# Performance work log

Hardware: AMD Instinct MI355X
Metric: run time of the kernel (lower is better)

The kernel has to match this reference:

```python
import jax, jax.numpy as jnp
import numpy as np

N = 100000
E = 1600000
DF = 64

def setup_inputs() -> dict:
    key = jax.random.key(0)
    ks = jax.random.split(key, 8)
    y = jax.random.normal(ks[0], (N, 3), dtype=jnp.float32)
    f_y = jax.random.normal(ks[1], (N, DF), dtype=jnp.float32)
    W0 = jax.random.normal(ks[2], (6, DF), dtype=jnp.float32) * 0.1
    b0 = jnp.zeros((DF,), dtype=jnp.float32)
    W1 = jax.random.normal(ks[3], (DF, DF), dtype=jnp.float32) * 0.1
    b1 = jnp.zeros((DF,), dtype=jnp.float32)
    neighbors_index = jax.random.randint(ks[4], (E,), 0, N, dtype=jnp.int64)
    # CSR row splits: sorted random interior split points, bracketed by 0 and E
    interior = jnp.sort(jax.random.randint(ks[5], (N - 1,), 0, E, dtype=jnp.int64))
    neighbors_row_splits = jnp.concatenate([
        jnp.zeros((1,), dtype=jnp.int64), interior,
        jnp.full((1,), E, dtype=jnp.int64)])
    return {"y": y, "f_y": f_y, "W0": W0, "b0": b0, "W1": W1, "b1": b1,
            "neighbors_index": neighbors_index,
            "neighbors_row_splits": neighbors_row_splits}

def reference(y, f_y, W0, b0, W1, b1, neighbors_index, neighbors_row_splits):
    n = y.shape[0]
    e = neighbors_index.shape[0]
    # segment id of each edge (inverse of CSR row splits), == repeat_interleave
    seg = jnp.searchsorted(neighbors_row_splits, jnp.arange(e, dtype=neighbors_row_splits.dtype), side='right') - 1
    rep_features = y[neighbors_index]          # [E, d1] neighbor coords
    self_features = y[seg]                     # [E, d2] self coords (x = y)
    agg = jnp.concatenate([rep_features, self_features], axis=1)  # [E, 6]
    # MLPLinear kernel: gelu between layers, none after last (torch gelu = exact erf)
    h = jax.nn.gelu(agg @ W0 + b0, approximate=False)
    h = h @ W1 + b1                            # [E, DF]
    # transform_type 0 -> (b): k(x,y) * f(y)
    h = h * f_y[neighbors_index]
    # segment_csr mean reduction (no weights)
    sums = jax.ops.segment_sum(h, seg, num_segments=n)            # [n, DF]
    counts = (neighbors_row_splits[1:] - neighbors_row_splits[:-1]).astype(h.dtype)
    out = sums / jnp.maximum(counts, 1.0)[:, None]
    return out
```

## Files before the change

kernel.cpp:

```cpp
#include <hip/hip_runtime.h>
#include <hip/hip_bf16.h>

#define NN    100000
#define EE    1600000
#define DF    64
#define BPB   5

typedef __bf16 bf16x8 __attribute__((ext_vector_type(8)));
typedef float  f32x4  __attribute__((ext_vector_type(4)));

__device__ __forceinline__ float gelu_f(float x) {
    float u2 = x * (2.302234849f + 0.102953097f * x * x);
    float s  = exp2f(-u2);
    return __fdividef(x, 1.0f + s);
}

__device__ __forceinline__ unsigned cvt_pk_bf16(float lo, float hi) {
    unsigned r;
    asm("v_cvt_pk_bf16_f32 %0, %1, %2" : "=v"(r) : "v"(lo), "v"(hi));
    return r;
}

__global__ void it_seg(const int* __restrict__ splits, int* __restrict__ seg) {
    const int e0 = (blockIdx.x * 256 + threadIdx.x) * 2;
    int n = 0;
    #pragma unroll
    for (int step = 65536; step >= 1; step >>= 1) {
        const int cand = n + step;
        if (cand <= NN - 1 && splits[cand] <= e0) n = cand;
    }
    int2 s;
    s.x = n;
    const int e1 = e0 + 1;
    while (n < NN - 1 && splits[n + 1] <= e1) n++;
    s.y = n;
    *(int2*)(seg + e0) = s;
}

__global__ __launch_bounds__(256, 4)
void it_edge(const float* __restrict__ y, const float* __restrict__ fy,
             const float* __restrict__ W0, const float* __restrict__ b0,
             const float* __restrict__ W1, const float* __restrict__ b1,
             const int* __restrict__ nbr, const int* __restrict__ seg,
             __bf16* __restrict__ h)
{
    __shared__ __align__(16) int    nbL[4][64];
    __shared__ __align__(16) __bf16 aggW[4][64][8];
    __shared__ __align__(16) __bf16 hL[4][16][DF];

    const int t    = threadIdx.x;
    const int lane = t & 63;
    const int wv   = t >> 6;
    const int col  = lane & 15;
    const int kg   = lane >> 4;

    bf16x8 w0f[4];
    #pragma unroll
    for (int nt = 0; nt < 4; nt++)
        #pragma unroll
        for (int j = 0; j < 8; j++) {
            const int k = kg * 8 + j;
            float v = 0.0f;
            if (k < 6)       v = W0[k * DF + nt * 16 + col];
            else if (k == 6) v = b0[nt * 16 + col];
            w0f[nt][j] = (__bf16)v;
        }
    bf16x8 w1f[4][2];
    float  b1r[4];
    #pragma unroll
    for (int nt = 0; nt < 4; nt++) {
        b1r[nt] = b1[col * 4 + nt];
        #pragma unroll
        for (int kf = 0; kf < 2; kf++)
            #pragma unroll
            for (int j = 0; j < 8; j++)
                w1f[nt][kf][j] = (__bf16)W1[(kf * 32 + kg * 8 + j) * DF + col * 4 + nt];
    }

    __bf16* const hw = &hL[wv][0][0];
    const int swz = (col & 7) << 4;

    #pragma unroll 1
    for (int bb = 0; bb < BPB; bb++) {
        const int ebase = (blockIdx.x * BPB + bb) * 256 + wv * 64;
        const int e     = ebase + lane;
        const int nb    = nbr[e];
        const int sge   = seg[e];
        nbL[wv][lane] = nb;
        bf16x8 ag = {};
        ag[0] = (__bf16)y[nb * 3 + 0];
        ag[1] = (__bf16)y[nb * 3 + 1];
        ag[2] = (__bf16)y[nb * 3 + 2];
        ag[3] = (__bf16)y[sge * 3 + 0];
        ag[4] = (__bf16)y[sge * 3 + 1];
        ag[5] = (__bf16)y[sge * 3 + 2];
        ag[6] = (__bf16)1.0f;
        *(bf16x8*)&aggW[wv][lane][0] = ag;

        #pragma unroll
        for (int g = 0; g < 4; g++) {
            const int gb = g * 16;
            const int4 q = *(const int4*)&nbL[wv][gb + kg * 4];

            bf16x8 a0 = {};
            if (kg == 0) a0 = *(const bf16x8*)&aggW[wv][gb + col][0];

            f32x4 acc0[4] = {};
            #pragma unroll
            for (int nt = 0; nt < 4; nt++)
                acc0[nt] = __builtin_amdgcn_mfma_f32_16x16x32_bf16(w0f[nt], a0, acc0[nt], 0, 0, 0);

            #pragma unroll
            for (int nt = 0; nt < 4; nt++) {
                const unsigned p0 = cvt_pk_bf16(gelu_f(acc0[nt][0]), gelu_f(acc0[nt][1]));
                const unsigned p1 = cvt_pk_bf16(gelu_f(acc0[nt][2]), gelu_f(acc0[nt][3]));
                const int off = col * 128 + ((nt * 32 + kg * 8) ^ swz);
                *(int2*)((char*)hw + off) = make_int2((int)p0, (int)p1);
            }
            bf16x8 af1[2];
            #pragma unroll
            for (int kf = 0; kf < 2; kf++) {
                const int off = col * 128 + ((kf * 64 + kg * 16) ^ swz);
                af1[kf] = *(const bf16x8*)((const char*)hw + off);
            }

            f32x4 acc[4] = {};
            #pragma unroll
            for (int nt = 0; nt < 4; nt++) {
                acc[nt] = __builtin_amdgcn_mfma_f32_16x16x32_bf16(af1[0], w1f[nt][0], acc[nt], 0, 0, 0);
                acc[nt] = __builtin_amdgcn_mfma_f32_16x16x32_bf16(af1[1], w1f[nt][1], acc[nt], 0, 0, 0);
            }

            #pragma unroll
            for (int r = 0; r < 4; r++) {
                const int qq = (&q.x)[r];
                const float4 fv = *(const float4*)(fy + (size_t)qq * DF + col * 4);
                const unsigned u0 = cvt_pk_bf16((acc[0][r] + b1r[0]) * fv.x,
                                                (acc[1][r] + b1r[1]) * fv.y);
                const unsigned u1 = cvt_pk_bf16((acc[2][r] + b1r[2]) * fv.z,
                                                (acc[3][r] + b1r[3]) * fv.w);
                const size_t er = (size_t)(ebase + gb + kg * 4 + r);
                *(int2*)((char*)h + er * 128 + col * 8) = make_int2((int)u0, (int)u1);
            }
        }
    }
}

__global__ void it_reduce(const int* __restrict__ splits,
                          const __bf16* __restrict__ h,
                          float* __restrict__ out)
{
    const int t    = threadIdx.x;
    const int lane = t & 63;
    const int wv   = t >> 6;
    const int n    = blockIdx.x * 4 + wv;
    const int s0 = splits[n], s1 = splits[n + 1];
    const int par = lane >> 4;
    const int cp  = lane & 15;

    float a0 = 0.f, a1 = 0.f, a2 = 0.f, a3 = 0.f;
    for (int e = s0 + par; e < s1; e += 4) {
        const unsigned long long u =
            *(const unsigned long long*)((const char*)h + (size_t)e * 128 + cp * 8);
        const unsigned lo = (unsigned)u, hi = (unsigned)(u >> 32);
        a0 += __uint_as_float(lo << 16);
        a1 += __uint_as_float(lo & 0xffff0000u);
        a2 += __uint_as_float(hi << 16);
        a3 += __uint_as_float(hi & 0xffff0000u);
    }
    a0 += __shfl_xor(a0, 16); a0 += __shfl_xor(a0, 32);
    a1 += __shfl_xor(a1, 16); a1 += __shfl_xor(a1, 32);
    a2 += __shfl_xor(a2, 16); a2 += __shfl_xor(a2, 32);
    a3 += __shfl_xor(a3, 16); a3 += __shfl_xor(a3, 32);

    if (lane < 16) {
        const int cnt = s1 - s0;
        const float inv = (cnt > 0) ? __fdividef(1.0f, (float)cnt) : 0.0f;
        float4 v; v.x = a0 * inv; v.y = a1 * inv; v.z = a2 * inv; v.w = a3 * inv;
        *(float4*)(out + (size_t)n * DF + cp * 4) = v;
    }
}


extern "C" void kernel_launch(void* const* d_in, const int* in_sizes, int n_in,
                              void* d_out, int out_size, void* d_ws, size_t ws_size,
                              hipStream_t stream) {
    const float* y   = (const float*)d_in[0];
    const float* fyv = (const float*)d_in[1];
    const float* W0  = (const float*)d_in[2];
    const float* b0  = (const float*)d_in[3];
    const float* W1  = (const float*)d_in[4];
    const float* b1  = (const float*)d_in[5];
    const int*   nb  = (const int*)d_in[6];
    const int*   sp  = (const int*)d_in[7];

    const size_t SEG_BYTES = (size_t)EE * 4;
    int*    seg = (int*)d_ws;
    __bf16* h   = (__bf16*)((char*)d_ws + SEG_BYTES);

    it_seg   <<<EE / 512,         256, 0, stream>>>(sp, seg);
    it_edge  <<<EE / (256 * BPB), 256, 0, stream>>>(y, fyv, W0, b0, W1, b1, nb, seg, h);
    it_reduce<<<NN / 4,           256, 0, stream>>>(sp, h, (float*)d_out);
}
```

Baseline: 176.9 us.

## Fuse segment-mean reduction into edge kernel via float atomics into output

Drops the bf16 per-edge intermediate buffer and the separate CSR reduce kernel. The edge kernel now scales each edge by a precomputed 1/count and atomically adds into a zeroed fp32 output. When four consecutive edges share a segment they are pre-summed, giving one atomic per column instead of four. This removes the write and re-read of the large intermediate, at the cost of many global atomics, a memset, and a twice-as-large segment/inverse-count workspace.

```diff
diff --git a/kernel.cpp b/kernel.cpp
--- a/kernel.cpp
+++ b/kernel.cpp
@@ -21,7 +21,7 @@
     return r;
 }
 
-__global__ void it_seg(const int* __restrict__ splits, int* __restrict__ seg) {
+__global__ void it_seg(const int* __restrict__ splits, int2* __restrict__ seg2) {
     const int e0 = (blockIdx.x * 256 + threadIdx.x) * 2;
     int n = 0;
     #pragma unroll
@@ -29,22 +29,28 @@
         const int cand = n + step;
         if (cand <= NN - 1 && splits[cand] <= e0) n = cand;
     }
-    int2 s;
-    s.x = n;
+    const int n0 = n;
+    const float i0 = __fdividef(1.0f, (float)(splits[n0 + 1] - splits[n0]));
     const int e1 = e0 + 1;
     while (n < NN - 1 && splits[n + 1] <= e1) n++;
-    s.y = n;
-    *(int2*)(seg + e0) = s;
+    const float i1 = (n == n0) ? i0
+                   : __fdividef(1.0f, (float)(splits[n + 1] - splits[n]));
+    int4 s;
+    s.x = n0; s.y = __float_as_int(i0);
+    s.z = n;  s.w = __float_as_int(i1);
+    *(int4*)(seg2 + e0) = s;
 }
 
 __global__ __launch_bounds__(256, 4)
-void it_edge(const float* __restrict__ y, const float* __restrict__ fy,
-             const float* __restrict__ W0, const float* __restrict__ b0,
-             const float* __restrict__ W1, const float* __restrict__ b1,
-             const int* __restrict__ nbr, const int* __restrict__ seg,
-             __bf16* __restrict__ h)
+void it_edge_at(const float* __restrict__ y, const float* __restrict__ fy,
+                const float* __restrict__ W0, const float* __restrict__ b0,
+                const float* __restrict__ W1, const float* __restrict__ b1,
+                const int* __restrict__ nbr, const int2* __restrict__ seg2,
+                float* __restrict__ out)
 {
-    __shared__ __align__(16) int    nbL[4][64];
+    __shared__ __align__(16) int    nbA[4][64];
+    __shared__ __align__(16) int    sgA[4][64];
+    __shared__ __align__(16) float  ivA[4][64];
     __shared__ __align__(16) __bf16 aggW[4][64][8];
     __shared__ __align__(16) __bf16 hL[4][16][DF];
 
@@ -82,25 +88,29 @@
 
     #pragma unroll 1
     for (int bb = 0; bb < BPB; bb++) {
-        const int ebase = (blockIdx.x * BPB + bb) * 256 + wv * 64;
-        const int e     = ebase + lane;
-        const int nb    = nbr[e];
-        const int sge   = seg[e];
-        nbL[wv][lane] = nb;
+        const int e   = (blockIdx.x * BPB + bb) * 256 + wv * 64 + lane;
+        const int nb  = nbr[e];
+        const int2 s2 = seg2[e];
+        nbA[wv][lane] = nb;
+        sgA[wv][lane] = s2.x;
+        ivA[wv][lane] = __int_as_float(s2.y);
         bf16x8 ag = {};
         ag[0] = (__bf16)y[nb * 3 + 0];
         ag[1] = (__bf16)y[nb * 3 + 1];
         ag[2] = (__bf16)y[nb * 3 + 2];
-        ag[3] = (__bf16)y[sge * 3 + 0];
-        ag[4] = (__bf16)y[sge * 3 + 1];
-        ag[5] = (__bf16)y[sge * 3 + 2];
+        ag[3] = (__bf16)y[s2.x * 3 + 0];
+        ag[4] = (__bf16)y[s2.x * 3 + 1];
+        ag[5] = (__bf16)y[s2.x * 3 + 2];
         ag[6] = (__bf16)1.0f;
         *(bf16x8*)&aggW[wv][lane][0] = ag;
 
         #pragma unroll
         for (int g = 0; g < 4; g++) {
             const int gb = g * 16;
-            const int4 q = *(const int4*)&nbL[wv][gb + kg * 4];
+            const int qi = gb + kg * 4;
+            const int4   nb4 = *(const int4*)&nbA[wv][qi];
+            const int4   sg4 = *(const int4*)&sgA[wv][qi];
+            const float4 iv4 = *(const float4*)&ivA[wv][qi];
 
             bf16x8 a0 = {};
             if (kg == 0) a0 = *(const bf16x8*)&aggW[wv][gb + col][0];
@@ -124,60 +134,40 @@
                 af1[kf] = *(const bf16x8*)((const char*)hw + off);
             }
 
-            f32x4 acc[4] = {};
+            f32x4 acc[4];
             #pragma unroll
             for (int nt = 0; nt < 4; nt++) {
+                const float bb1 = b1r[nt];
+                acc[nt][0] = bb1; acc[nt][1] = bb1; acc[nt][2] = bb1; acc[nt][3] = bb1;
                 acc[nt] = __builtin_amdgcn_mfma_f32_16x16x32_bf16(af1[0], w1f[nt][0], acc[nt], 0, 0, 0);
                 acc[nt] = __builtin_amdgcn_mfma_f32_16x16x32_bf16(af1[1], w1f[nt][1], acc[nt], 0, 0, 0);
             }
 
             #pragma unroll
             for (int r = 0; r < 4; r++) {
-                const int qq = (&q.x)[r];
-                const float4 fv = *(const float4*)(fy + (size_t)qq * DF + col * 4);
-                const unsigned u0 = cvt_pk_bf16((acc[0][r] + b1r[0]) * fv.x,
-                                                (acc[1][r] + b1r[1]) * fv.y);
-                const unsigned u1 = cvt_pk_bf16((acc[2][r] + b1r[2]) * fv.z,
-                                                (acc[3][r] + b1r[3]) * fv.w);
-                const size_t er = (size_t)(ebase + gb + kg * 4 + r);
-                *(int2*)((char*)h + er * 128 + col * 8) = make_int2((int)u0, (int)u1);
+                const float4 fv = *(const float4*)(fy + (size_t)(&nb4.x)[r] * DF + col * 4);
+                const float  iv = (&iv4.x)[r];
+                #pragma unroll
+                for (int nt = 0; nt < 4; nt++)
+                    acc[nt][r] = acc[nt][r] * ((&fv.x)[nt] * iv);
+            }
+
+            if (sg4.x == sg4.w) {
+                float* const op = out + (size_t)sg4.x * DF + col * 4;
+                #pragma unroll
+                for (int nt = 0; nt < 4; nt++)
+                    unsafeAtomicAdd(op + nt,
+                        (acc[nt][0] + acc[nt][1]) + (acc[nt][2] + acc[nt][3]));
+            } else {
+                #pragma unroll
+                for (int r = 0; r < 4; r++) {
+                    float* const op = out + (size_t)(&sg4.x)[r] * DF + col * 4;
+                    #pragma unroll
+                    for (int nt = 0; nt < 4; nt++)
+                        unsafeAtomicAdd(op + nt, acc[nt][r]);
+                }
             }
         }
-    }
-}
-
-__global__ void it_reduce(const int* __restrict__ splits,
-                          const __bf16* __restrict__ h,
-                          float* __restrict__ out)
-{
-    const int t    = threadIdx.x;
-    const int lane = t & 63;
-    const int wv   = t >> 6;
-    const int n    = blockIdx.x * 4 + wv;
-    const int s0 = splits[n], s1 = splits[n + 1];
-    const int par = lane >> 4;
-    const int cp  = lane & 15;
-
-    float a0 = 0.f, a1 = 0.f, a2 = 0.f, a3 = 0.f;
-    for (int e = s0 + par; e < s1; e += 4) {
-        const unsigned long long u =
-            *(const unsigned long long*)((const char*)h + (size_t)e * 128 + cp * 8);
-        const unsigned lo = (unsigned)u, hi = (unsigned)(u >> 32);
-        a0 += __uint_as_float(lo << 16);
-        a1 += __uint_as_float(lo & 0xffff0000u);
-        a2 += __uint_as_float(hi << 16);
-        a3 += __uint_as_float(hi & 0xffff0000u);
-    }
-    a0 += __shfl_xor(a0, 16); a0 += __shfl_xor(a0, 32);
-    a1 += __shfl_xor(a1, 16); a1 += __shfl_xor(a1, 32);
-    a2 += __shfl_xor(a2, 16); a2 += __shfl_xor(a2, 32);
-    a3 += __shfl_xor(a3, 16); a3 += __shfl_xor(a3, 32);
-
-    if (lane < 16) {
-        const int cnt = s1 - s0;
-        const float inv = (cnt > 0) ? __fdividef(1.0f, (float)cnt) : 0.0f;
-        float4 v; v.x = a0 * inv; v.y = a1 * inv; v.z = a2 * inv; v.w = a3 * inv;
-        *(float4*)(out + (size_t)n * DF + cp * 4) = v;
     }
 }
 
@@ -194,11 +184,10 @@
     const int*   nb  = (const int*)d_in[6];
     const int*   sp  = (const int*)d_in[7];
 
-    const size_t SEG_BYTES = (size_t)EE * 4;
-    int*    seg = (int*)d_ws;
-    __bf16* h   = (__bf16*)((char*)d_ws + SEG_BYTES);
+    int2* seg2 = (int2*)d_ws;
+    float* out = (float*)d_out;
 
-    it_seg   <<<EE / 512,         256, 0, stream>>>(sp, seg);
-    it_edge  <<<EE / (256 * BPB), 256, 0, stream>>>(y, fyv, W0, b0, W1, b1, nb, seg, h);
-    it_reduce<<<NN / 4,           256, 0, stream>>>(sp, h, (float*)d_out);
+    hipMemsetAsync(out, 0, (size_t)NN * DF * sizeof(float), stream);
+    it_seg    <<<EE / 512, 256, 0, stream>>>(sp, seg2);
+    it_edge_at<<<EE / (256 * BPB), 256, 0, stream>>>(y, fyv, W0, b0, W1, b1, nb, seg2, out);
 }
```

Measured after the change: 691.6 us. +291.0%, slower.

## Use persistent edge kernel with atomic work-stealing batch counter and fold b1 into MFMA init

Applied to the files above, without the earlier changes.

The edge kernel becomes persistent: a fixed grid of 1536 blocks pulls 256-edge batches from a global atomic counter, double-buffering the next batch index in shared memory, with a block barrier per batch. This replaces the static assignment of five batches per block, aiming to balance load and reduce tail effects. The b1 bias is now used as the initial MFMA accumulator instead of being added afterwards. The counter is stored in the last float of the output buffer, zeroed with a memset and later overwritten by the reduce kernel. This adds an extra memset, one atomic per batch and a __syncthreads per batch.

```diff
diff --git a/kernel.cpp b/kernel.cpp
--- a/kernel.cpp
+++ b/kernel.cpp
@@ -1,10 +1,11 @@
 #include <hip/hip_runtime.h>
 #include <hip/hip_bf16.h>
 
-#define NN    100000
-#define EE    1600000
-#define DF    64
-#define BPB   5
+#define NN      100000
+#define EE      1600000
+#define DF      64
+#define NBATCH  (EE / 256)
+#define GRID_E  1536
 
 typedef __bf16 bf16x8 __attribute__((ext_vector_type(8)));
 typedef float  f32x4  __attribute__((ext_vector_type(4)));
@@ -42,11 +43,12 @@
              const float* __restrict__ W0, const float* __restrict__ b0,
              const float* __restrict__ W1, const float* __restrict__ b1,
              const int* __restrict__ nbr, const int* __restrict__ seg,
-             __bf16* __restrict__ h)
+             int* __restrict__ counter, __bf16* __restrict__ h)
 {
     __shared__ __align__(16) int    nbL[4][64];
     __shared__ __align__(16) __bf16 aggW[4][64][8];
     __shared__ __align__(16) __bf16 hL[4][16][DF];
+    __shared__ int batL[2];
 
     const int t    = threadIdx.x;
     const int lane = t & 63;
@@ -80,9 +82,15 @@
     __bf16* const hw = &hL[wv][0][0];
     const int swz = (col & 7) << 4;
 
-    #pragma unroll 1
-    for (int bb = 0; bb < BPB; bb++) {
-        const int ebase = (blockIdx.x * BPB + bb) * 256 + wv * 64;
+    if (t == 0) batL[0] = atomicAdd(counter, 1);
+    __syncthreads();
+
+    for (int it = 0; ; it++) {
+        const int bat = batL[it & 1];
+        if (bat >= NBATCH) break;
+        if (t == 0) batL[(it + 1) & 1] = atomicAdd(counter, 1);
+
+        const int ebase = bat * 256 + wv * 64;
         const int e     = ebase + lane;
         const int nb    = nbr[e];
         const int sge   = seg[e];
@@ -124,9 +132,11 @@
                 af1[kf] = *(const bf16x8*)((const char*)hw + off);
             }
 
-            f32x4 acc[4] = {};
+            f32x4 acc[4];
             #pragma unroll
             for (int nt = 0; nt < 4; nt++) {
+                const float bb1 = b1r[nt];
+                acc[nt][0] = bb1; acc[nt][1] = bb1; acc[nt][2] = bb1; acc[nt][3] = bb1;
                 acc[nt] = __builtin_amdgcn_mfma_f32_16x16x32_bf16(af1[0], w1f[nt][0], acc[nt], 0, 0, 0);
                 acc[nt] = __builtin_amdgcn_mfma_f32_16x16x32_bf16(af1[1], w1f[nt][1], acc[nt], 0, 0, 0);
             }
@@ -135,14 +145,14 @@
             for (int r = 0; r < 4; r++) {
                 const int qq = (&q.x)[r];
                 const float4 fv = *(const float4*)(fy + (size_t)qq * DF + col * 4);
-                const unsigned u0 = cvt_pk_bf16((acc[0][r] + b1r[0]) * fv.x,
-                                                (acc[1][r] + b1r[1]) * fv.y);
-                const unsigned u1 = cvt_pk_bf16((acc[2][r] + b1r[2]) * fv.z,
-                                                (acc[3][r] + b1r[3]) * fv.w);
+                const unsigned u0 = cvt_pk_bf16(acc[0][r] * fv.x, acc[1][r] * fv.y);
+                const unsigned u1 = cvt_pk_bf16(acc[2][r] * fv.z, acc[3][r] * fv.w);
                 const size_t er = (size_t)(ebase + gb + kg * 4 + r);
                 *(int2*)((char*)h + er * 128 + col * 8) = make_int2((int)u0, (int)u1);
             }
         }
+
+        __syncthreads();
     }
 }
 
@@ -198,7 +208,10 @@
     int*    seg = (int*)d_ws;
     __bf16* h   = (__bf16*)((char*)d_ws + SEG_BYTES);
 
-    it_seg   <<<EE / 512,         256, 0, stream>>>(sp, seg);
-    it_edge  <<<EE / (256 * BPB), 256, 0, stream>>>(y, fyv, W0, b0, W1, b1, nb, seg, h);
-    it_reduce<<<NN / 4,           256, 0, stream>>>(sp, h, (float*)d_out);
-}
+    int* counter = (int*)((char*)d_out + (size_t)(NN * DF - 1) * 4);
+
+    hipMemsetAsync(counter, 0, 4, stream);
+    it_seg   <<<EE / 512, 256, 0, stream>>>(sp, seg);
+    it_edge  <<<GRID_E,   256, 0, stream>>>(y, fyv, W0, b0, W1, b1, nb, seg, counter, h);
+    it_reduce<<<NN / 4,   256, 0, stream>>>(sp, h, (float*)d_out);
+}
```

After: 195.8 us. +10.7%, slower.
